# Kernel optimization log

Hardware: AMD Instinct MI355X
Metric: run time of the kernel (lower is better)

The kernel has to match this reference:

```python
import jax, jax.numpy as jnp
import numpy as np

H, D, DK, DV = 8, 512, 64, 64
B, L = 2, 2048
LN_EPS = 1e-5


def setup_inputs() -> dict:
    key = jax.random.key(0)
    ks = jax.random.split(key, 12)
    q = jax.random.normal(ks[0], (B, L, D), jnp.float32)
    k = jax.random.normal(ks[1], (B, L, D), jnp.float32)
    v = jax.random.normal(ks[2], (B, L, D), jnp.float32)
    mask = jax.random.randint(ks[3], (H * B, L, L), 0, 2) > 0
    sq = np.sqrt(2.0 / (D + DK)).astype(np.float32)
    sv = np.sqrt(2.0 / (D + DV)).astype(np.float32)
    Wq = jax.random.normal(ks[4], (H * DK, D), jnp.float32) * sq
    Wk = jax.random.normal(ks[5], (H * DK, D), jnp.float32) * sq
    Wv = jax.random.normal(ks[6], (H * DV, D), jnp.float32) * sv
    xav = np.sqrt(2.0 / (H * DV + D)).astype(np.float32)
    Wfc = jax.random.normal(ks[7], (D, H * DV), jnp.float32) * xav
    bfc = jnp.zeros((D,), jnp.float32)
    gamma = jnp.ones((D,), jnp.float32)
    beta = jnp.zeros((D,), jnp.float32)
    return {"q": q, "k": k, "v": v, "mask": mask, "Wq": Wq, "Wk": Wk,
            "Wv": Wv, "Wfc": Wfc, "bfc": bfc, "gamma": gamma, "beta": beta}


def reference(q, k, v, mask, Wq, Wk, Wv, Wfc, bfc, gamma, beta):
    # dropout in eval mode (identity)
    temperature = jnp.sqrt(jnp.asarray(DK, q.dtype))
    residual = q
    # projections -> (H, B, L, dk/dv), matching permute(2,0,1,3)
    qh = (q @ Wq.T).reshape(B, L, H, DK).transpose(2, 0, 1, 3)
    kh = (k @ Wk.T).reshape(B, L, H, DK).transpose(2, 0, 1, 3)
    vh = (v @ Wv.T).reshape(B, L, H, DV).transpose(2, 0, 1, 3)
    attn = jnp.einsum('hbqd,hbkd->hbqk', qh, kh) / temperature
    m = mask.reshape(H, B, L, L)
    attn = jnp.where(m, jnp.asarray(-1e10, attn.dtype), attn)
    attn = jax.nn.softmax(attn, axis=-1)
    out = jnp.einsum('hbqk,hbkd->hbqd', attn, vh)  # (H,B,L,DV)
    out = out.transpose(1, 2, 0, 3).reshape(B, L, H * DV)
    out = out @ Wfc.T + bfc
    x = out + residual
    mu = jnp.mean(x, axis=-1, keepdims=True)
    var = jnp.var(x, axis=-1, keepdims=True)
    return gamma * (x - mu) * jax.lax.rsqrt(var + LN_EPS) + beta
```

## Files before the change

kernel.cpp:

```cpp
#include <hip/hip_runtime.h>
#include <hip/hip_bf16.h>
#include <cmath>
#include <cstdint>

#define H_ 8
#define B_ 2
#define L_ 2048
#define D_ 512
#define SPLIT_ 4

typedef __attribute__((ext_vector_type(8))) short short8_t;
typedef __attribute__((ext_vector_type(4))) float float4_t;
typedef __attribute__((ext_vector_type(4))) unsigned short ushort4_t;
typedef __attribute__((ext_vector_type(4))) unsigned int uint4_t;

__device__ __forceinline__ unsigned short bf16u(float f) {
  union { __hip_bfloat16 b; unsigned short u; } c;
  c.b = __float2bfloat16(f);
  return c.u;
}
__device__ __forceinline__ unsigned bf16x2(float lo, float hi) {
  return (unsigned)bf16u(lo) | ((unsigned)bf16u(hi) << 16);
}
__device__ __forceinline__ float bf2f(unsigned short u) {
  union { unsigned u; float f; } c; c.u = (unsigned)u << 16; return c.f;
}

__device__ __forceinline__ unsigned pack8(unsigned long long x) {
  x |= x >> 4; x |= x >> 2; x |= x >> 1;
  x &= 0x0101010101010101ULL;
  return (unsigned)((x * 0x0102040810204080ULL) >> 56);
}

__global__ __launch_bounds__(512)
void proj_gemm(const float* __restrict__ q, const float* __restrict__ k,
               const float* __restrict__ v,
               const float* __restrict__ wq, const float* __restrict__ wk,
               const float* __restrict__ wv,
               unsigned short* __restrict__ Qp, unsigned short* __restrict__ Kp,
               unsigned short* __restrict__ Vt) {
  __shared__ unsigned short As[128][72];
  __shared__ unsigned short Bs[64][72];
  const int tid = threadIdx.x, lane = tid & 63, wave = tid >> 6;
  const int g = lane >> 4, qi = lane & 15;
  const int m0 = blockIdx.x * 128, n0 = blockIdx.y * 64;
  const int z = blockIdx.z;
  const float* A = (z == 0) ? q : (z == 1) ? k : v;
  const float* W = (z == 0) ? wq : (z == 1) ? wk : wv;

  float4_t acc[4] = {};
  const int ar = tid >> 2, ac = (tid & 3) * 16;
  const int br = tid >> 3, bc = (tid & 7) * 8;

  for (int kt = 0; kt < 512; kt += 64) {
    const float* src = A + (size_t)(m0 + ar) * 512 + kt + ac;
    float4_t f0 = *(const float4_t*)(src);
    float4_t f1 = *(const float4_t*)(src + 4);
    float4_t f2 = *(const float4_t*)(src + 8);
    float4_t f3 = *(const float4_t*)(src + 12);
    short8_t s0, s1;
    s0[0] = bf16u(f0[0]); s0[1] = bf16u(f0[1]); s0[2] = bf16u(f0[2]); s0[3] = bf16u(f0[3]);
    s0[4] = bf16u(f1[0]); s0[5] = bf16u(f1[1]); s0[6] = bf16u(f1[2]); s0[7] = bf16u(f1[3]);
    s1[0] = bf16u(f2[0]); s1[1] = bf16u(f2[1]); s1[2] = bf16u(f2[2]); s1[3] = bf16u(f2[3]);
    s1[4] = bf16u(f3[0]); s1[5] = bf16u(f3[1]); s1[6] = bf16u(f3[2]); s1[7] = bf16u(f3[3]);
    *(short8_t*)(&As[ar][ac]) = s0;
    *(short8_t*)(&As[ar][ac + 8]) = s1;
    const float* wsrc = W + (size_t)(n0 + br) * 512 + kt + bc;
    float4_t w0 = *(const float4_t*)(wsrc);
    float4_t w1 = *(const float4_t*)(wsrc + 4);
    short8_t sw;
    sw[0] = bf16u(w0[0]); sw[1] = bf16u(w0[1]); sw[2] = bf16u(w0[2]); sw[3] = bf16u(w0[3]);
    sw[4] = bf16u(w1[0]); sw[5] = bf16u(w1[1]); sw[6] = bf16u(w1[2]); sw[7] = bf16u(w1[3]);
    *(short8_t*)(&Bs[br][bc]) = sw;
    __syncthreads();
#pragma unroll
    for (int kk = 0; kk < 2; kk++) {
      const int krow = kk * 32 + g * 8;
      short8_t a = *(const short8_t*)(&As[wave * 16 + qi][krow]);
#pragma unroll
      for (int n = 0; n < 4; n++) {
        short8_t b = *(const short8_t*)(&Bs[n * 16 + qi][krow]);
        acc[n] = __builtin_amdgcn_mfma_f32_16x16x32_bf16(a, b, acc[n], 0, 0, 0);
      }
    }
    __syncthreads();
  }

  const int gmb = m0 + wave * 16 + g * 4;
#pragma unroll
  for (int n = 0; n < 4; n++) {
    int gn = n0 + n * 16 + qi;
    int h = gn >> 6, d = gn & 63;
    if (z == 2) {
      int bb = gmb >> 11, l = gmb & 2047;
      ushort4_t o;
#pragma unroll
      for (int r = 0; r < 4; r++) o[r] = bf16u(acc[n][r]);
      *(ushort4_t*)(Vt + ((size_t)(h * B_ + bb) * 64 + d) * L_ + l) = o;
    } else {
      float sc = (z == 0) ? 0.125f : 1.0f;
      unsigned short* O = (z == 0) ? Qp : Kp;
#pragma unroll
      for (int r = 0; r < 4; r++) {
        int gm = gmb + r;
        int bb = gm >> 11, l = gm & 2047;
        O[((size_t)(h * B_ + bb) * L_ + l) * 64 + d] = bf16u(acc[n][r] * sc);
      }
    }
  }
}

template<int MS>
__device__ __forceinline__ void attn_body(
    const unsigned short* __restrict__ Qp, const unsigned short* __restrict__ Kp,
    const unsigned short* __restrict__ Vt, const unsigned char* __restrict__ mask,
    unsigned short* __restrict__ Opart, float* __restrict__ MLpart,
    unsigned short (*Ks)[64][72], unsigned short (*Vs)[64][72]) {
  const int tid = threadIdx.x, lane = tid & 63, wave = tid >> 6;
  const int g = lane >> 4, qi = lane & 15;
  const int hb = blockIdx.y;
  const int sp = blockIdx.z;
  const int k_begin = sp * (L_ / SPLIT_), k_end = k_begin + L_ / SPLIT_;
  const int qg0 = blockIdx.x * 128 + wave * 16;
  const int qg = qg0 + qi;
  const size_t base = (size_t)hb * (L_ * 64);

  const size_t mrowoff = ((size_t)hb * L_ + qg0 + (lane >> 2)) * L_;
  const unsigned char* mb1 = mask + mrowoff + (lane & 3) * 16;
  const unsigned* mb4 = (const unsigned*)mask + mrowoff + (lane & 3) * 16;

  short8_t qf[2];
#pragma unroll
  for (int kk = 0; kk < 2; kk++)
    qf[kk] = *(const short8_t*)(Qp + base + (size_t)qg * 64 + kk * 32 + g * 8);

  float4_t o[4] = {};
  float mrun = -INFINITY, lrun = 0.f;
  const int sr = tid >> 3, sc = (tid & 7) * 8;
  const int srcA = qi * 4;
  const int srcP = qi + 32 * (g & 1);

#define LOADFB(dst, kpos)                                                        \
  do {                                                                           \
    if (MS == 1) {                                                               \
      uint4_t x = *(const uint4_t*)(mb1 + (kpos));                               \
      unsigned long long lo = ((unsigned long long)x[1] << 32) | x[0];           \
      unsigned long long hi = ((unsigned long long)x[3] << 32) | x[2];           \
      dst = pack8(lo) | (pack8(hi) << 8);                                        \
    } else {                                                                     \
      dst = 0;                                                                   \
      _Pragma("unroll")                                                          \
      for (int j = 0; j < 4; j++) {                                              \
        uint4_t x = *(const uint4_t*)(mb4 + (kpos) + j * 4);                     \
        dst |= (((unsigned)(x[0] != 0)) | ((unsigned)(x[1] != 0) << 1) |         \
                ((unsigned)(x[2] != 0) << 2) | ((unsigned)(x[3] != 0) << 3))     \
               << (j * 4);                                                       \
      }                                                                          \
    }                                                                            \
  } while (0)

  short8_t kr, vr;
  unsigned fb1, fb2;
  kr = *(const short8_t*)(Kp + base + (size_t)(k_begin + sr) * 64 + sc);
  vr = *(const short8_t*)(Vt + base + (size_t)sr * L_ + k_begin + sc);
  LOADFB(fb1, k_begin);
  fb2 = 0;
  if (k_begin + 64 < k_end) LOADFB(fb2, k_begin + 64);
  *(short8_t*)(&Ks[0][sr][sc]) = kr;
  *(short8_t*)(&Vs[0][sr][sc]) = vr;
  __syncthreads();

  int bufi = 0;
  for (int k0 = k_begin; k0 < k_end; k0 += 64) {
    const bool has_next = (k0 + 64 < k_end);
    if (has_next) {
      const int kn = k0 + 64;
      kr = *(const short8_t*)(Kp + base + (size_t)(kn + sr) * 64 + sc);
      vr = *(const short8_t*)(Vt + base + (size_t)sr * L_ + kn + sc);
    }
    unsigned fb_cur = fb1;
    fb1 = fb2;
    if (k0 + 128 < k_end) LOADFB(fb2, k0 + 128);

    unsigned nib[4];
#pragma unroll
    for (int t = 0; t < 4; t++)
      nib[t] = ((unsigned)__shfl((int)fb_cur, srcA + t, 64) >> (g * 4)) & 0xFu;

    float4_t st[4] = {};
#pragma unroll
    for (int kk = 0; kk < 2; kk++) {
      const int krow = kk * 32 + g * 8;
#pragma unroll
      for (int t = 0; t < 4; t++) {
        short8_t a = *(const short8_t*)(&Ks[bufi][t * 16 + qi][krow]);
        st[t] = __builtin_amdgcn_mfma_f32_16x16x32_bf16(a, qf[kk], st[t], 0, 0, 0);
      }
    }

    float tmax = -INFINITY;
#pragma unroll
    for (int t = 0; t < 4; t++)
#pragma unroll
      for (int r = 0; r < 4; r++) {
        if ((nib[t] >> r) & 1u) st[t][r] = -1e10f;
        tmax = fmaxf(tmax, st[t][r]);
      }
    tmax = fmaxf(tmax, __shfl_xor(tmax, 16, 64));
    tmax = fmaxf(tmax, __shfl_xor(tmax, 32, 64));

    float nm = fmaxf(mrun, tmax);
    float fac = __expf(mrun - nm);
    mrun = nm;

    float psum = 0.f;
    unsigned w8[4][2];
#pragma unroll
    for (int t = 0; t < 4; t++) {
      float p0 = __expf(st[t][0] - nm);
      float p1 = __expf(st[t][1] - nm);
      float p2 = __expf(st[t][2] - nm);
      float p3 = __expf(st[t][3] - nm);
      psum += (p0 + p1) + (p2 + p3);
      w8[t][0] = bf16x2(p0, p1);
      w8[t][1] = bf16x2(p2, p3);
    }
    psum += __shfl_xor(psum, 16, 64);
    psum += __shfl_xor(psum, 32, 64);
    lrun = lrun * fac + psum;
#pragma unroll
    for (int n2 = 0; n2 < 4; n2++)
#pragma unroll
      for (int r = 0; r < 4; r++) o[n2][r] *= fac;

#pragma unroll
    for (int s = 0; s < 2; s++) {
      unsigned a00 = (unsigned)__shfl((int)w8[2 * s][0],     srcP, 64);
      unsigned a10 = (unsigned)__shfl((int)w8[2 * s + 1][0], srcP, 64);
      unsigned a01 = (unsigned)__shfl((int)w8[2 * s][1],     srcP, 64);
      unsigned a11 = (unsigned)__shfl((int)w8[2 * s + 1][1], srcP, 64);
      unsigned b00 = (unsigned)__shfl((int)w8[2 * s][0],     srcP + 16, 64);
      unsigned b10 = (unsigned)__shfl((int)w8[2 * s + 1][0], srcP + 16, 64);
      unsigned b01 = (unsigned)__shfl((int)w8[2 * s][1],     srcP + 16, 64);
      unsigned b11 = (unsigned)__shfl((int)w8[2 * s + 1][1], srcP + 16, 64);
      const bool hi = (g & 2) != 0;
      union { unsigned u[4]; short8_t s8; } pb;
      pb.u[0] = hi ? a10 : a00;
      pb.u[1] = hi ? a11 : a01;
      pb.u[2] = hi ? b10 : b00;
      pb.u[3] = hi ? b11 : b01;
#pragma unroll
      for (int n2 = 0; n2 < 4; n2++) {
        short8_t a = *(const short8_t*)(&Vs[bufi][n2 * 16 + qi][s * 32 + g * 8]);
        o[n2] = __builtin_amdgcn_mfma_f32_16x16x32_bf16(a, pb.s8, o[n2], 0, 0, 0);
      }
    }

    if (has_next) {
      *(short8_t*)(&Ks[bufi ^ 1][sr][sc]) = kr;
      *(short8_t*)(&Vs[bufi ^ 1][sr][sc]) = vr;
      __syncthreads();
      bufi ^= 1;
    }
  }
#undef LOADFB

  const size_t pb = (((size_t)sp * 16 + hb) * L_ + qg) * 64;
#pragma unroll
  for (int n2 = 0; n2 < 4; n2++) {
    ushort4_t ov;
#pragma unroll
    for (int r = 0; r < 4; r++) ov[r] = bf16u(o[n2][r]);
    *(ushort4_t*)(Opart + pb + n2 * 16 + g * 4) = ov;
  }
  if (lane < 16) {
    float* ml = MLpart + (((size_t)sp * 16 + hb) * L_ + qg) * 2;
    ml[0] = mrun; ml[1] = lrun;
  }
}

__global__ __launch_bounds__(512)
void attn_split(const unsigned short* __restrict__ Qp, const unsigned short* __restrict__ Kp,
                const unsigned short* __restrict__ Vt, const unsigned char* __restrict__ mask,
                unsigned short* __restrict__ Opart, float* __restrict__ MLpart) {
  __shared__ unsigned short Ks[2][64][72];
  __shared__ unsigned short Vs[2][64][72];
  unsigned probe = ((const unsigned*)mask)[threadIdx.x & 63];
  if (__any(probe > 1u))
    attn_body<1>(Qp, Kp, Vt, mask, Opart, MLpart, Ks, Vs);
  else
    attn_body<4>(Qp, Kp, Vt, mask, Opart, MLpart, Ks, Vs);
}

__global__ __launch_bounds__(256)
void attn_combine(const unsigned short* __restrict__ Opart, const float* __restrict__ MLpart,
                  unsigned short* __restrict__ Y) {
  int gid = blockIdx.x * 256 + threadIdx.x;
  int dvc = (gid & 7) * 8;
  int hbq = gid >> 3;
  int hb = hbq >> 11, qq = hbq & 2047;
  int h = hb >> 1, bb = hb & 1;
  float m[SPLIT_], l[SPLIT_];
  float M = -INFINITY;
#pragma unroll
  for (int s = 0; s < SPLIT_; s++) {
    const float* ml = MLpart + (((size_t)s * 16 + hb) * L_ + qq) * 2;
    m[s] = ml[0]; l[s] = ml[1];
    M = fmaxf(M, m[s]);
  }
  float denom = 0.f, e[SPLIT_];
#pragma unroll
  for (int s = 0; s < SPLIT_; s++) { e[s] = __expf(m[s] - M); denom += l[s] * e[s]; }
  float inv = 1.0f / denom;
  float acc[8] = {};
#pragma unroll
  for (int s = 0; s < SPLIT_; s++) {
    const unsigned short* p = Opart + (((size_t)s * 16 + hb) * L_ + qq) * 64 + dvc;
    ushort4_t a0 = *(const ushort4_t*)(p);
    ushort4_t a1 = *(const ushort4_t*)(p + 4);
    float w = e[s] * inv;
#pragma unroll
    for (int j = 0; j < 4; j++) {
      acc[j] += bf2f(a0[j]) * w;
      acc[j + 4] += bf2f(a1[j]) * w;
    }
  }
  short8_t ov;
#pragma unroll
  for (int j = 0; j < 8; j++) ov[j] = bf16u(acc[j]);
  *(short8_t*)(Y + ((size_t)(bb * L_ + qq)) * 512 + h * 64 + dvc) = ov;
}

__global__ __launch_bounds__(512)
void fc_gemm(const unsigned short* __restrict__ Yb, const float* __restrict__ wfc,
             const float* __restrict__ resid, const float* __restrict__ bfc,
             float* __restrict__ out) {
  __shared__ unsigned short As[128][72];
  __shared__ unsigned short Bs[64][72];
  const int tid = threadIdx.x, lane = tid & 63, wave = tid >> 6;
  const int g = lane >> 4, qi = lane & 15;
  const int m0 = blockIdx.x * 128, n0 = blockIdx.y * 64;
  float4_t acc[4] = {};
  const int ar = tid >> 2, ac = (tid & 3) * 16;
  const int br = tid >> 3, bc = (tid & 7) * 8;

  for (int kt = 0; kt < 512; kt += 64) {
    const unsigned short* src = Yb + (size_t)(m0 + ar) * 512 + kt + ac;
    *(short8_t*)(&As[ar][ac]) = *(const short8_t*)(src);
    *(short8_t*)(&As[ar][ac + 8]) = *(const short8_t*)(src + 8);
    const float* wsrc = wfc + (size_t)(n0 + br) * 512 + kt + bc;
    float4_t w0 = *(const float4_t*)(wsrc);
    float4_t w1 = *(const float4_t*)(wsrc + 4);
    short8_t sw;
    sw[0] = bf16u(w0[0]); sw[1] = bf16u(w0[1]); sw[2] = bf16u(w0[2]); sw[3] = bf16u(w0[3]);
    sw[4] = bf16u(w1[0]); sw[5] = bf16u(w1[1]); sw[6] = bf16u(w1[2]); sw[7] = bf16u(w1[3]);
    *(short8_t*)(&Bs[br][bc]) = sw;
    __syncthreads();
#pragma unroll
    for (int kk = 0; kk < 2; kk++) {
      const int krow = kk * 32 + g * 8;
      short8_t a = *(const short8_t*)(&As[wave * 16 + qi][krow]);
#pragma unroll
      for (int n = 0; n < 4; n++) {
        short8_t b = *(const short8_t*)(&Bs[n * 16 + qi][krow]);
        acc[n] = __builtin_amdgcn_mfma_f32_16x16x32_bf16(a, b, acc[n], 0, 0, 0);
      }
    }
    __syncthreads();
  }

  const int gmb = m0 + wave * 16 + g * 4;
#pragma unroll
  for (int n = 0; n < 4; n++) {
    int gn = n0 + n * 16 + qi;
    float bv = bfc[gn];
#pragma unroll
    for (int r = 0; r < 4; r++) {
      int gm = gmb + r;
      out[(size_t)gm * 512 + gn] = acc[n][r] + bv + resid[(size_t)gm * 512 + gn];
    }
  }
}

__global__ __launch_bounds__(256)
void ln_kernel(float* __restrict__ Z, const float* __restrict__ gamma,
               const float* __restrict__ beta) {
  const int row = blockIdx.x * 4 + (threadIdx.x >> 6);
  const int lane = threadIdx.x & 63;
  float* zp = Z + (size_t)row * 512 + lane * 8;
  float4_t x0 = *(const float4_t*)(zp);
  float4_t x1 = *(const float4_t*)(zp + 4);
  float s = 0.f, s2 = 0.f;
#pragma unroll
  for (int j = 0; j < 4; j++) { s += x0[j] + x1[j]; s2 += x0[j] * x0[j] + x1[j] * x1[j]; }
#pragma unroll
  for (int mm = 1; mm < 64; mm <<= 1) { s += __shfl_xor(s, mm, 64); s2 += __shfl_xor(s2, mm, 64); }
  float mu = s * (1.f / 512.f);
  float var = s2 * (1.f / 512.f) - mu * mu;
  float inv = rsqrtf(var + 1e-5f);
  float4_t g0 = *(const float4_t*)(gamma + lane * 8);
  float4_t g1 = *(const float4_t*)(gamma + lane * 8 + 4);
  float4_t b0 = *(const float4_t*)(beta + lane * 8);
  float4_t b1 = *(const float4_t*)(beta + lane * 8 + 4);
#pragma unroll
  for (int j = 0; j < 4; j++) {
    x0[j] = g0[j] * (x0[j] - mu) * inv + b0[j];
    x1[j] = g1[j] * (x1[j] - mu) * inv + b1[j];
  }
  *(float4_t*)(zp) = x0;
  *(float4_t*)(zp + 4) = x1;
}

extern "C" void kernel_launch(void* const* d_in, const int* in_sizes, int n_in,
                              void* d_out, int out_size, void* d_ws, size_t ws_size,
                              hipStream_t stream) {
  const float* q   = (const float*)d_in[0];
  const float* k   = (const float*)d_in[1];
  const float* v   = (const float*)d_in[2];
  const unsigned char* mask = (const unsigned char*)d_in[3];
  const float* Wq  = (const float*)d_in[4];
  const float* Wk  = (const float*)d_in[5];
  const float* Wv  = (const float*)d_in[6];
  const float* Wfc = (const float*)d_in[7];
  const float* bfc = (const float*)d_in[8];
  const float* gamma = (const float*)d_in[9];
  const float* beta  = (const float*)d_in[10];
  float* out = (float*)d_out;

  char* ws = (char*)d_ws;
  unsigned short* Qp   = (unsigned short*)(ws);
  unsigned short* Kp   = Qp + 2097152;
  unsigned short* Vt   = Kp + 2097152;
  unsigned short* Y    = Vt + 2097152;
  unsigned short* Opart = Y + 2097152;
  float* MLpart = (float*)(Opart + (size_t)SPLIT_ * 16 * L_ * 64);

  proj_gemm<<<dim3(32, 8, 3), 512, 0, stream>>>(q, k, v, Wq, Wk, Wv, Qp, Kp, Vt);
  attn_split<<<dim3(16, 16, SPLIT_), 512, 0, stream>>>(Qp, Kp, Vt, mask, Opart, MLpart);
  attn_combine<<<1024, 256, 0, stream>>>(Opart, MLpart, Y);
  fc_gemm<<<dim3(32, 8), 512, 0, stream>>>(Y, Wfc, q, bfc, out);
  ln_kernel<<<1024, 256, 0, stream>>>(out, gamma, beta);
}
```

Measured before the change: 123.3 us.

## Process two query tiles per wave and route P through LDS

Each wave now handles 32 query rows as two 16-row tiles, so every K/V LDS fragment read feeds two MFMAs. The grid's query dimension is halved to match, and the mask bit-packing is widened to 32 bits per lane. The P matrix is no longer moved into the MFMA B-operand layout with many cross-lane shuffles; it is written to a per-wave LDS scratch and read back. This adds register pressure and about 36KB of LDS, and leaves fewer blocks (512 instead of 1024) to fill the GPU, which can hurt occupancy.

Result: slower. 139.2 us (+12.8%).

```diff
diff --git a/kernel.cpp b/kernel.cpp
--- a/kernel.cpp
+++ b/kernel.cpp
@@ -12,6 +12,7 @@
 typedef __attribute__((ext_vector_type(8))) short short8_t;
 typedef __attribute__((ext_vector_type(4))) float float4_t;
 typedef __attribute__((ext_vector_type(4))) unsigned short ushort4_t;
+typedef __attribute__((ext_vector_type(2))) unsigned int uint2_t;
 typedef __attribute__((ext_vector_type(4))) unsigned int uint4_t;
 
 __device__ __forceinline__ unsigned short bf16u(float f) {
@@ -115,42 +116,48 @@
     const unsigned short* __restrict__ Qp, const unsigned short* __restrict__ Kp,
     const unsigned short* __restrict__ Vt, const unsigned char* __restrict__ mask,
     unsigned short* __restrict__ Opart, float* __restrict__ MLpart,
-    unsigned short (*Ks)[64][72], unsigned short (*Vs)[64][72]) {
+    unsigned short (*Ks)[64][72], unsigned short (*Vs)[64][72],
+    unsigned int (*Ps)[72]) {
   const int tid = threadIdx.x, lane = tid & 63, wave = tid >> 6;
   const int g = lane >> 4, qi = lane & 15;
   const int hb = blockIdx.y;
   const int sp = blockIdx.z;
   const int k_begin = sp * (L_ / SPLIT_), k_end = k_begin + L_ / SPLIT_;
-  const int qg0 = blockIdx.x * 128 + wave * 16;
-  const int qg = qg0 + qi;
+  const int qg0 = blockIdx.x * 256 + wave * 32;
+  const int qgA = qg0 + qi, qgB = qg0 + 16 + qi;
   const size_t base = (size_t)hb * (L_ * 64);
 
-  const size_t mrowoff = ((size_t)hb * L_ + qg0 + (lane >> 2)) * L_;
-  const unsigned char* mb1 = mask + mrowoff + (lane & 3) * 16;
-  const unsigned* mb4 = (const unsigned*)mask + mrowoff + (lane & 3) * 16;
-
-  short8_t qf[2];
-#pragma unroll
-  for (int kk = 0; kk < 2; kk++)
-    qf[kk] = *(const short8_t*)(Qp + base + (size_t)qg * 64 + kk * 32 + g * 8);
-
-  float4_t o[4] = {};
-  float mrun = -INFINITY, lrun = 0.f;
+  const size_t mrowoff = ((size_t)hb * L_ + qg0 + (lane >> 1)) * L_;
+  const unsigned char* mb1 = mask + mrowoff + (lane & 1) * 32;
+  const unsigned* mb4 = (const unsigned*)mask + mrowoff + (lane & 1) * 32;
+
+  short8_t qfA[2], qfB[2];
+#pragma unroll
+  for (int kk = 0; kk < 2; kk++) {
+    qfA[kk] = *(const short8_t*)(Qp + base + (size_t)qgA * 64 + kk * 32 + g * 8);
+    qfB[kk] = *(const short8_t*)(Qp + base + (size_t)qgB * 64 + kk * 32 + g * 8);
+  }
+
+  float4_t oA[4] = {}, oB[4] = {};
+  float mrA = -INFINITY, lrA = 0.f, mrB = -INFINITY, lrB = 0.f;
   const int sr = tid >> 3, sc = (tid & 7) * 8;
-  const int srcA = qi * 4;
-  const int srcP = qi + 32 * (g & 1);
+  const int srcA = 2 * qi;
+  const int srcB = 32 + 2 * qi;
 
 #define LOADFB(dst, kpos)                                                        \
   do {                                                                           \
     if (MS == 1) {                                                               \
-      uint4_t x = *(const uint4_t*)(mb1 + (kpos));                               \
-      unsigned long long lo = ((unsigned long long)x[1] << 32) | x[0];           \
-      unsigned long long hi = ((unsigned long long)x[3] << 32) | x[2];           \
-      dst = pack8(lo) | (pack8(hi) << 8);                                        \
+      uint4_t x0_ = *(const uint4_t*)(mb1 + (kpos));                             \
+      uint4_t x1_ = *(const uint4_t*)(mb1 + (kpos) + 16);                        \
+      unsigned long long q0_ = ((unsigned long long)x0_[1] << 32) | x0_[0];      \
+      unsigned long long q1_ = ((unsigned long long)x0_[3] << 32) | x0_[2];      \
+      unsigned long long q2_ = ((unsigned long long)x1_[1] << 32) | x1_[0];      \
+      unsigned long long q3_ = ((unsigned long long)x1_[3] << 32) | x1_[2];      \
+      dst = pack8(q0_) | (pack8(q1_) << 8) | (pack8(q2_) << 16) | (pack8(q3_) << 24); \
     } else {                                                                     \
       dst = 0;                                                                   \
       _Pragma("unroll")                                                          \
-      for (int j = 0; j < 4; j++) {                                              \
+      for (int j = 0; j < 8; j++) {                                              \
         uint4_t x = *(const uint4_t*)(mb4 + (kpos) + j * 4);                     \
         dst |= (((unsigned)(x[0] != 0)) | ((unsigned)(x[1] != 0) << 1) |         \
                 ((unsigned)(x[2] != 0) << 2) | ((unsigned)(x[3] != 0) << 3))     \
@@ -182,77 +189,101 @@
     fb1 = fb2;
     if (k0 + 128 < k_end) LOADFB(fb2, k0 + 128);
 
-    unsigned nib[4];
-#pragma unroll
-    for (int t = 0; t < 4; t++)
-      nib[t] = ((unsigned)__shfl((int)fb_cur, srcA + t, 64) >> (g * 4)) & 0xFu;
-
-    float4_t st[4] = {};
+    unsigned nibA[4], nibB[4];
+#pragma unroll
+    for (int t = 0; t < 4; t++) {
+      nibA[t] = ((unsigned)__shfl((int)fb_cur, srcA + (t >> 1), 64) >> (16 * (t & 1) + 4 * g)) & 0xFu;
+      nibB[t] = ((unsigned)__shfl((int)fb_cur, srcB + (t >> 1), 64) >> (16 * (t & 1) + 4 * g)) & 0xFu;
+    }
+
+    float4_t stA[4] = {}, stB[4] = {};
 #pragma unroll
     for (int kk = 0; kk < 2; kk++) {
       const int krow = kk * 32 + g * 8;
 #pragma unroll
       for (int t = 0; t < 4; t++) {
         short8_t a = *(const short8_t*)(&Ks[bufi][t * 16 + qi][krow]);
-        st[t] = __builtin_amdgcn_mfma_f32_16x16x32_bf16(a, qf[kk], st[t], 0, 0, 0);
-      }
-    }
-
-    float tmax = -INFINITY;
-#pragma unroll
-    for (int t = 0; t < 4; t++)
-#pragma unroll
-      for (int r = 0; r < 4; r++) {
-        if ((nib[t] >> r) & 1u) st[t][r] = -1e10f;
-        tmax = fmaxf(tmax, st[t][r]);
-      }
-    tmax = fmaxf(tmax, __shfl_xor(tmax, 16, 64));
-    tmax = fmaxf(tmax, __shfl_xor(tmax, 32, 64));
-
-    float nm = fmaxf(mrun, tmax);
-    float fac = __expf(mrun - nm);
-    mrun = nm;
-
-    float psum = 0.f;
-    unsigned w8[4][2];
-#pragma unroll
-    for (int t = 0; t < 4; t++) {
-      float p0 = __expf(st[t][0] - nm);
-      float p1 = __expf(st[t][1] - nm);
-      float p2 = __expf(st[t][2] - nm);
-      float p3 = __expf(st[t][3] - nm);
-      psum += (p0 + p1) + (p2 + p3);
-      w8[t][0] = bf16x2(p0, p1);
-      w8[t][1] = bf16x2(p2, p3);
-    }
-    psum += __shfl_xor(psum, 16, 64);
-    psum += __shfl_xor(psum, 32, 64);
-    lrun = lrun * fac + psum;
-#pragma unroll
-    for (int n2 = 0; n2 < 4; n2++)
-#pragma unroll
-      for (int r = 0; r < 4; r++) o[n2][r] *= fac;
+        stA[t] = __builtin_amdgcn_mfma_f32_16x16x32_bf16(a, qfA[kk], stA[t], 0, 0, 0);
+        stB[t] = __builtin_amdgcn_mfma_f32_16x16x32_bf16(a, qfB[kk], stB[t], 0, 0, 0);
+      }
+    }
+
+    {
+      float tmax = -INFINITY;
+#pragma unroll
+      for (int t = 0; t < 4; t++)
+#pragma unroll
+        for (int r = 0; r < 4; r++) {
+          if ((nibA[t] >> r) & 1u) stA[t][r] = -1e10f;
+          tmax = fmaxf(tmax, stA[t][r]);
+        }
+      tmax = fmaxf(tmax, __shfl_xor(tmax, 16, 64));
+      tmax = fmaxf(tmax, __shfl_xor(tmax, 32, 64));
+      float nm = fmaxf(mrA, tmax);
+      float fac = __expf(mrA - nm);
+      mrA = nm;
+      float psum = 0.f;
+#pragma unroll
+      for (int t = 0; t < 4; t++) {
+        float p0 = __expf(stA[t][0] - nm);
+        float p1 = __expf(stA[t][1] - nm);
+        float p2 = __expf(stA[t][2] - nm);
+        float p3 = __expf(stA[t][3] - nm);
+        psum += (p0 + p1) + (p2 + p3);
+        uint2_t w2; w2[0] = bf16x2(p0, p1); w2[1] = bf16x2(p2, p3);
+        *(uint2_t*)(&Ps[qi][t * 8 + g * 2]) = w2;
+      }
+      psum += __shfl_xor(psum, 16, 64);
+      psum += __shfl_xor(psum, 32, 64);
+      lrA = lrA * fac + psum;
+#pragma unroll
+      for (int n2 = 0; n2 < 4; n2++)
+#pragma unroll
+        for (int r = 0; r < 4; r++) oA[n2][r] *= fac;
+    }
+    {
+      float tmax = -INFINITY;
+#pragma unroll
+      for (int t = 0; t < 4; t++)
+#pragma unroll
+        for (int r = 0; r < 4; r++) {
+          if ((nibB[t] >> r) & 1u) stB[t][r] = -1e10f;
+          tmax = fmaxf(tmax, stB[t][r]);
+        }
+      tmax = fmaxf(tmax, __shfl_xor(tmax, 16, 64));
+      tmax = fmaxf(tmax, __shfl_xor(tmax, 32, 64));
+      float nm = fmaxf(mrB, tmax);
+      float fac = __expf(mrB - nm);
+      mrB = nm;
+      float psum = 0.f;
+#pragma unroll
+      for (int t = 0; t < 4; t++) {
+        float p0 = __expf(stB[t][0] - nm);
+        float p1 = __expf(stB[t][1] - nm);
+        float p2 = __expf(stB[t][2] - nm);
+        float p3 = __expf(stB[t][3] - nm);
+        psum += (p0 + p1) + (p2 + p3);
+        uint2_t w2; w2[0] = bf16x2(p0, p1); w2[1] = bf16x2(p2, p3);
+        *(uint2_t*)(&Ps[qi][36 + t * 8 + g * 2]) = w2;
+      }
+      psum += __shfl_xor(psum, 16, 64);
+      psum += __shfl_xor(psum, 32, 64);
+      lrB = lrB * fac + psum;
+#pragma unroll
+      for (int n2 = 0; n2 < 4; n2++)
+#pragma unroll
+        for (int r = 0; r < 4; r++) oB[n2][r] *= fac;
+    }
 
 #pragma unroll
     for (int s = 0; s < 2; s++) {
-      unsigned a00 = (unsigned)__shfl((int)w8[2 * s][0],     srcP, 64);
-      unsigned a10 = (unsigned)__shfl((int)w8[2 * s + 1][0], srcP, 64);
-      unsigned a01 = (unsigned)__shfl((int)w8[2 * s][1],     srcP, 64);
-      unsigned a11 = (unsigned)__shfl((int)w8[2 * s + 1][1], srcP, 64);
-      unsigned b00 = (unsigned)__shfl((int)w8[2 * s][0],     srcP + 16, 64);
-      unsigned b10 = (unsigned)__shfl((int)w8[2 * s + 1][0], srcP + 16, 64);
-      unsigned b01 = (unsigned)__shfl((int)w8[2 * s][1],     srcP + 16, 64);
-      unsigned b11 = (unsigned)__shfl((int)w8[2 * s + 1][1], srcP + 16, 64);
-      const bool hi = (g & 2) != 0;
-      union { unsigned u[4]; short8_t s8; } pb;
-      pb.u[0] = hi ? a10 : a00;
-      pb.u[1] = hi ? a11 : a01;
-      pb.u[2] = hi ? b10 : b00;
-      pb.u[3] = hi ? b11 : b01;
+      short8_t pbA = *(const short8_t*)(&Ps[qi][s * 16 + g * 4]);
+      short8_t pbB = *(const short8_t*)(&Ps[qi][36 + s * 16 + g * 4]);
 #pragma unroll
       for (int n2 = 0; n2 < 4; n2++) {
         short8_t a = *(const short8_t*)(&Vs[bufi][n2 * 16 + qi][s * 32 + g * 8]);
-        o[n2] = __builtin_amdgcn_mfma_f32_16x16x32_bf16(a, pb.s8, o[n2], 0, 0, 0);
+        oA[n2] = __builtin_amdgcn_mfma_f32_16x16x32_bf16(a, pbA, oA[n2], 0, 0, 0);
+        oB[n2] = __builtin_amdgcn_mfma_f32_16x16x32_bf16(a, pbB, oB[n2], 0, 0, 0);
       }
     }
 
@@ -265,17 +296,22 @@
   }
 #undef LOADFB
 
-  const size_t pb = (((size_t)sp * 16 + hb) * L_ + qg) * 64;
+  const size_t pbA_ = (((size_t)sp * 16 + hb) * L_ + qgA) * 64;
+  const size_t pbB_ = (((size_t)sp * 16 + hb) * L_ + qgB) * 64;
 #pragma unroll
   for (int n2 = 0; n2 < 4; n2++) {
-    ushort4_t ov;
-#pragma unroll
-    for (int r = 0; r < 4; r++) ov[r] = bf16u(o[n2][r]);
-    *(ushort4_t*)(Opart + pb + n2 * 16 + g * 4) = ov;
+    ushort4_t ovA, ovB;
+#pragma unroll
+    for (int r = 0; r < 4; r++) { ovA[r] = bf16u(oA[n2][r]); ovB[r] = bf16u(oB[n2][r]); }
+    *(ushort4_t*)(Opart + pbA_ + n2 * 16 + g * 4) = ovA;
+    *(ushort4_t*)(Opart + pbB_ + n2 * 16 + g * 4) = ovB;
   }
   if (lane < 16) {
-    float* ml = MLpart + (((size_t)sp * 16 + hb) * L_ + qg) * 2;
-    ml[0] = mrun; ml[1] = lrun;
+    float* ml = MLpart + (((size_t)sp * 16 + hb) * L_ + qg0 + lane) * 2;
+    ml[0] = mrA; ml[1] = lrA;
+  } else if (lane < 32) {
+    float* ml = MLpart + (((size_t)sp * 16 + hb) * L_ + qg0 + 16 + (lane & 15)) * 2;
+    ml[0] = mrB; ml[1] = lrB;
   }
 }
 
@@ -285,11 +321,13 @@
                 unsigned short* __restrict__ Opart, float* __restrict__ MLpart) {
   __shared__ unsigned short Ks[2][64][72];
   __shared__ unsigned short Vs[2][64][72];
+  __shared__ unsigned int PsAll[8][16][72];
+  const int wave = threadIdx.x >> 6;
   unsigned probe = ((const unsigned*)mask)[threadIdx.x & 63];
   if (__any(probe > 1u))
-    attn_body<1>(Qp, Kp, Vt, mask, Opart, MLpart, Ks, Vs);
+    attn_body<1>(Qp, Kp, Vt, mask, Opart, MLpart, Ks, Vs, PsAll[wave]);
   else
-    attn_body<4>(Qp, Kp, Vt, mask, Opart, MLpart, Ks, Vs);
+    attn_body<4>(Qp, Kp, Vt, mask, Opart, MLpart, Ks, Vs, PsAll[wave]);
 }
 
 __global__ __launch_bounds__(256)
@@ -436,7 +474,7 @@
   float* MLpart = (float*)(Opart + (size_t)SPLIT_ * 16 * L_ * 64);
 
   proj_gemm<<<dim3(32, 8, 3), 512, 0, stream>>>(q, k, v, Wq, Wk, Wv, Qp, Kp, Vt);
-  attn_split<<<dim3(16, 16, SPLIT_), 512, 0, stream>>>(Qp, Kp, Vt, mask, Opart, MLpart);
+  attn_split<<<dim3(8, 16, SPLIT_), 512, 0, stream>>>(Qp, Kp, Vt, mask, Opart, MLpart);
   attn_combine<<<1024, 256, 0, stream>>>(Opart, MLpart, Y);
   fc_gemm<<<dim3(32, 8), 512, 0, stream>>>(Y, Wfc, q, bfc, out);
   ln_kernel<<<1024, 256, 0, stream>>>(out, gamma, beta);
```
